# Kernel optimization log

Hardware: AMD Instinct MI355X
Metric: run time of the kernel (lower is better)

The kernel has to match this reference:

```python
import jax, jax.numpy as jnp
import numpy as np

H = 8
DA, DP, DK = 2048, 1024, 1024
B, N = 4, 2048
DOUT = 512
INNER = (DA + DP + DK) // H  # 512 = heads*dim_head


def setup_inputs() -> dict:
    key = jax.random.key(0)
    ks = jax.random.split(key, 7)
    x = jax.random.normal(ks[0], (B, N, DA + DP + DK), jnp.float32)
    mask = jax.random.randint(ks[1], (B, 1, N, N), 0, 2, jnp.int32)
    W_a = jax.random.normal(ks[2], (3 * DA // H, DA), jnp.float32) * (DA ** -0.5)
    W_p = jax.random.normal(ks[3], (3 * DP // H, DP), jnp.float32) * (DP ** -0.5)
    W_k = jax.random.normal(ks[4], (3 * DK // H, DK), jnp.float32) * (DK ** -0.5)
    W_out = jax.random.normal(ks[5], (DOUT, INNER), jnp.float32) * (INNER ** -0.5)
    b_out = jnp.zeros((DOUT,), jnp.float32)
    return {"x": x, "W_a": W_a, "W_p": W_p, "W_k": W_k,
            "W_out": W_out, "b_out": b_out, "mask": mask}


def _heads(t):  # [b, n, h*d] -> [b, h, n, d]
    b, n, hd = t.shape
    return t.reshape(b, n, H, hd // H).transpose(0, 2, 1, 3)


def reference(x, W_a, W_p, W_k, W_out, b_out, mask):
    # three branch QKV projections (each branch sees its own slice of x)
    qkv_a = x[..., :DA] @ W_a.T                      # [b, n, 3*DA/H]
    qkv_p = x[..., DA:DA + DP] @ W_p.T               # [b, n, 3*DP/H]
    qkv_k = x[..., DA + DP:] @ W_k.T                 # [b, n, 3*DK/H]
    q_a, k_a, v_a = [_heads(t) for t in jnp.split(qkv_a, 3, axis=-1)]
    q_p, k_p, v_p = [_heads(t) for t in jnp.split(qkv_p, 3, axis=-1)]
    q_k, k_k, v_k = [_heads(t) for t in jnp.split(qkv_k, 3, axis=-1)]

    m = mask > 0                                     # [b, 1, n, n]
    neg = jnp.asarray(-1e10, x.dtype)

    def branch(q, k, d):
        dots = jnp.einsum('bhid,bhjd->bhij', q, k) * (d ** -0.5)
        return jax.nn.softmax(jnp.where(m, dots, neg), axis=-1)

    # betas = [1,1,1] normalized -> 1/3 each (the nn.Parameters are unused in fwd)
    attn = (branch(q_a, k_a, DA) + branch(q_p, k_p, DP) + branch(q_k, k_k, DK)) / 3.0

    v = jnp.concatenate([v_a, v_p, v_k], axis=-1)    # [b, h, n, INNER/H]
    out = jnp.einsum('bhij,bhjd->bhid', attn, v)     # [b, h, n, INNER/H]
    out = out.transpose(0, 2, 1, 3).reshape(x.shape[0], x.shape[1], INNER)
    return out @ W_out.T + b_out
```

## Files before the change

### kernel.cpp

```cpp
#include <hip/hip_runtime.h>
#include <hip/hip_bf16.h>

typedef __attribute__((ext_vector_type(8))) __bf16 bf16x8;
typedef __attribute__((ext_vector_type(4))) float f32x4;
typedef unsigned short u16;
typedef unsigned int u32;
typedef unsigned long long u64;

__device__ __forceinline__ u32 cvtpk(float lo, float hi) {
  u32 r;
  asm("v_cvt_pk_bf16_f32 %0, %1, %2" : "=v"(r) : "v"(lo), "v"(hi));
  return r;
}
__device__ __forceinline__ float rexp2(float x) {
  float r;
  asm("v_exp_f32 %0, %1" : "=v"(r) : "v"(x));
  return r;
}
__device__ __forceinline__ void gl_lds16(const void* g, void* l) {
  __builtin_amdgcn_global_load_lds((const __attribute__((address_space(1))) void*)g,
                                   (__attribute__((address_space(3))) void*)l, 16, 0, 0);
}

__global__ __launch_bounds__(256) void prep_kernel(
    const float* __restrict__ x, u16* __restrict__ xb,
    const float* __restrict__ Wa, const float* __restrict__ Wp,
    const float* __restrict__ Wk, const float* __restrict__ Wo,
    u16* __restrict__ Wab, u16* __restrict__ Wpb,
    u16* __restrict__ Wkb, u16* __restrict__ Wob,
    const int* __restrict__ mask, u64* __restrict__ bits, int xblocks) {
  int bid = blockIdx.x;
  if (bid < xblocks) {
    const int idx = (bid * 256 + threadIdx.x) * 16;
    const float4 a0 = *(const float4*)(x + idx);
    const float4 a1 = *(const float4*)(x + idx + 4);
    const float4 a2 = *(const float4*)(x + idx + 8);
    const float4 a3 = *(const float4*)(x + idx + 12);
    uint4 t0, t1;
    t0.x = cvtpk(a0.x, a0.y); t0.y = cvtpk(a0.z, a0.w);
    t0.z = cvtpk(a1.x, a1.y); t0.w = cvtpk(a1.z, a1.w);
    t1.x = cvtpk(a2.x, a2.y); t1.y = cvtpk(a2.z, a2.w);
    t1.z = cvtpk(a3.x, a3.y); t1.w = cvtpk(a3.z, a3.w);
    *(uint4*)(xb + idx) = t0;
    *(uint4*)(xb + idx + 8) = t1;
    return;
  }
  bid -= xblocks;
  if (bid < 2560) {
    const float* s; u16* d; int base;
    if (bid < 1536)      { s = Wa; d = Wab; base = bid; }
    else if (bid < 1920) { s = Wp; d = Wpb; base = bid - 1536; }
    else if (bid < 2304) { s = Wk; d = Wkb; base = bid - 1920; }
    else                 { s = Wo; d = Wob; base = bid - 2304; }
    const int idx = (base * 256 + threadIdx.x) * 4;
    const float4 v = *(const float4*)(s + idx);
    *(uint2*)(d + idx) = make_uint2(cvtpk(v.x, v.y), cvtpk(v.z, v.w));
    return;
  }
  bid -= 2560;
  const int lane = threadIdx.x & 63;
  const long long gw = (long long)bid * 4 + (threadIdx.x >> 6);
  const long long nwaves = 1024LL * 4;
  const long long nwords = 16777216LL / 64;
  for (long long i = gw; i < nwords; i += nwaves) {
    const int m = mask[i * 64 + lane];
    const u64 bal = __ballot(m > 0);
    if (lane == 0) bits[i] = bal;
  }
}

__device__ __forceinline__ void qkv_store(
    float v0, float v1, float v2, float v3, int m_base, int c,
    int dhs, int seg, float fs,
    u16* __restrict__ Qb, u16* __restrict__ Kb, u16* __restrict__ Vt) {
  const int which = c >> (3 + dhs);
  const float f = (which == 0) ? fs : 1.0f;
  const u32 r01 = cvtpk(v0 * f, v1 * f);
  const u32 r23 = cvtpk(v2 * f, v3 * f);
  const u16 bvv[4] = {(u16)r01, (u16)(r01 >> 16), (u16)r23, (u16)(r23 >> 16)};
  const int hd_mask = (8 << dhs) - 1;
  const int r = c & hd_mask;
  const int hh = r >> dhs;
  const int d = r & ((1 << dhs) - 1);
  #pragma unroll
  for (int j = 0; j < 4; ++j) {
    const int m = m_base + j;
    const int bb = m >> 11, n = m & 2047;
    const size_t bhn = (size_t)(bb * 8 + hh) * 2048 + n;
    const u16 bv = bvv[j];
    if (which == 0)      Qb[bhn * 64 + seg + d] = bv;
    else if (which == 1) Kb[bhn * 64 + seg + d] = bv;
    else {
      const int nk6 = n & 63;
      const int pos = ((nk6 >> 5) << 5) | (((nk6 & 15) >> 2) << 3)
                    | ((nk6 & 3) << 1) | ((nk6 >> 4) & 1);
      Vt[((size_t)(bb * 8 + hh) * 64 + seg + d) * 2048 + (n & ~63) + pos] = bv;
    }
  }
}

__global__ __launch_bounds__(256) void qkv_gemm_kernel(
    const u16* __restrict__ xb, const u16* __restrict__ Wa,
    const u16* __restrict__ Wp, const u16* __restrict__ Wk,
    u16* __restrict__ Qb, u16* __restrict__ Kb, u16* __restrict__ Vt) {
  __shared__ u16 lA[64 * 64];
  __shared__ u16 lB[128 * 64];

  const int tid = threadIdx.x;
  const int w = tid >> 6, l = tid & 63;
  const int lr = l & 15, lg = l >> 4;

  const int wg = blockIdx.x;
  const int xcd = wg & 7;
  const int q = wg >> 3;
  const int mtl = q / 12, nt = q % 12;
  const int mt = (xcd << 4) + mtl;

  const u16* W; int xoff, Kd, col0, dhs, seg;
  if (nt < 6)      { W = Wa; xoff = 0;    Kd = 2048; col0 = nt * 128;       dhs = 5; seg = 0;  }
  else if (nt < 9) { W = Wp; xoff = 2048; Kd = 1024; col0 = (nt - 6) * 128; dhs = 4; seg = 32; }
  else             { W = Wk; xoff = 3072; Kd = 1024; col0 = (nt - 9) * 128; dhs = 4; seg = 48; }
  const float qscale = (dhs == 5) ? 0.031880107f : 0.045084220f;

  const int m0 = mt * 64;
  f32x4 acc[4][2] = {};
  const int ubase = tid & ~63;

  const int nk = Kd >> 6;
  #pragma unroll 1
  for (int kt = 0; kt < nk; ++kt) {
    const int k0 = kt << 6;
    #pragma unroll
    for (int i = 0; i < 2; ++i) {
      const int ch = i * 256 + tid;
      const int row = ch >> 3, c8 = (ch & 7) << 3;
      gl_lds16(xb + (size_t)(m0 + row) * 4096 + xoff + k0 + c8,
               lA + (size_t)(i * 256 + ubase) * 8);
    }
    #pragma unroll
    for (int i = 0; i < 4; ++i) {
      const int ch = i * 256 + tid;
      const int row = ch >> 3, c8 = (ch & 7) << 3;
      gl_lds16(W + (size_t)(col0 + row) * Kd + k0 + c8,
               lB + (size_t)(i * 256 + ubase) * 8);
    }
    __syncthreads();
    bf16x8 af[4][2], bfr[2][2];
    #pragma unroll
    for (int mi = 0; mi < 4; ++mi) {
      af[mi][0] = *(const bf16x8*)(lA + (mi * 16 + lr) * 64 + lg * 8);
      af[mi][1] = *(const bf16x8*)(lA + (mi * 16 + lr) * 64 + 32 + lg * 8);
    }
    #pragma unroll
    for (int ni = 0; ni < 2; ++ni) {
      bfr[ni][0] = *(const bf16x8*)(lB + (w * 32 + ni * 16 + lr) * 64 + lg * 8);
      bfr[ni][1] = *(const bf16x8*)(lB + (w * 32 + ni * 16 + lr) * 64 + 32 + lg * 8);
    }
    #pragma unroll
    for (int mi = 0; mi < 4; ++mi)
      #pragma unroll
      for (int ni = 0; ni < 2; ++ni) {
        acc[mi][ni] = __builtin_amdgcn_mfma_f32_16x16x32_bf16(af[mi][0], bfr[ni][0], acc[mi][ni], 0, 0, 0);
        acc[mi][ni] = __builtin_amdgcn_mfma_f32_16x16x32_bf16(af[mi][1], bfr[ni][1], acc[mi][ni], 0, 0, 0);
      }
    __syncthreads();
  }

  #pragma unroll
  for (int mi = 0; mi < 4; ++mi)
    #pragma unroll
    for (int ni = 0; ni < 2; ++ni)
      qkv_store(acc[mi][ni][0], acc[mi][ni][1], acc[mi][ni][2], acc[mi][ni][3],
                m0 + mi * 16 + lg * 4, col0 + w * 32 + ni * 16 + lr,
                dhs, seg, qscale, Qb, Kb, Vt);
}

__global__ __launch_bounds__(256) void qkv_gemm_f32_kernel(
    const float* __restrict__ x, const u16* __restrict__ Wa,
    const u16* __restrict__ Wp, const u16* __restrict__ Wk,
    u16* __restrict__ Qb, u16* __restrict__ Kb, u16* __restrict__ Vt) {
  __shared__ u16 lA[128 * 64];
  __shared__ u16 lB[128 * 64];

  const int tid = threadIdx.x;
  const int w = tid >> 6, l = tid & 63;
  const int lr = l & 15, lg = l >> 4;
  const int wr = w >> 1, wc = w & 1;

  const int wg = blockIdx.x;
  const int xcd = wg & 7;
  const int q = wg >> 3;
  const int mtl = q / 12, nt = q % 12;
  const int mt = (xcd << 3) + mtl;

  const u16* W; int xoff, Kd, col0, dhs, seg;
  if (nt < 6)      { W = Wa; xoff = 0;    Kd = 2048; col0 = nt * 128;       dhs = 5; seg = 0;  }
  else if (nt < 9) { W = Wp; xoff = 2048; Kd = 1024; col0 = (nt - 6) * 128; dhs = 4; seg = 32; }
  else             { W = Wk; xoff = 3072; Kd = 1024; col0 = (nt - 9) * 128; dhs = 4; seg = 48; }
  const float qscale = (dhs == 5) ? 0.031880107f : 0.045084220f;

  const int m0 = mt * 128;
  f32x4 acc[4][4] = {};
  const int ubase = tid & ~63;

  const int nk = Kd >> 6;
  #pragma unroll 1
  for (int kt = 0; kt < nk; ++kt) {
    const int k0 = kt << 6;
    #pragma unroll
    for (int i = 0; i < 4; ++i) {
      const int ch = i * 256 + tid;
      const int row = ch >> 3, c8 = (ch & 7) << 3;
      const float* src = x + (size_t)(m0 + row) * 4096 + xoff + k0 + c8;
      const float4 a0 = *(const float4*)(src);
      const float4 a1 = *(const float4*)(src + 4);
      uint4 t;
      t.x = cvtpk(a0.x, a0.y); t.y = cvtpk(a0.z, a0.w);
      t.z = cvtpk(a1.x, a1.y); t.w = cvtpk(a1.z, a1.w);
      *(uint4*)(lA + (size_t)row * 64 + c8) = t;
    }
    #pragma unroll
    for (int i = 0; i < 4; ++i) {
      const int ch = i * 256 + tid;
      const int row = ch >> 3, c8 = (ch & 7) << 3;
      gl_lds16(W + (size_t)(col0 + row) * Kd + k0 + c8,
               lB + (size_t)(i * 256 + ubase) * 8);
    }
    __syncthreads();
    bf16x8 af[4][2], bfr[4][2];
    #pragma unroll
    for (int mi = 0; mi < 4; ++mi) {
      af[mi][0] = *(const bf16x8*)(lA + (wr * 64 + mi * 16 + lr) * 64 + lg * 8);
      af[mi][1] = *(const bf16x8*)(lA + (wr * 64 + mi * 16 + lr) * 64 + 32 + lg * 8);
    }
    #pragma unroll
    for (int ni = 0; ni < 4; ++ni) {
      bfr[ni][0] = *(const bf16x8*)(lB + (wc * 64 + ni * 16 + lr) * 64 + lg * 8);
      bfr[ni][1] = *(const bf16x8*)(lB + (wc * 64 + ni * 16 + lr) * 64 + 32 + lg * 8);
    }
    #pragma unroll
    for (int mi = 0; mi < 4; ++mi)
      #pragma unroll
      for (int ni = 0; ni < 4; ++ni) {
        acc[mi][ni] = __builtin_amdgcn_mfma_f32_16x16x32_bf16(af[mi][0], bfr[ni][0], acc[mi][ni], 0, 0, 0);
        acc[mi][ni] = __builtin_amdgcn_mfma_f32_16x16x32_bf16(af[mi][1], bfr[ni][1], acc[mi][ni], 0, 0, 0);
      }
    __syncthreads();
  }
  #pragma unroll
  for (int mi = 0; mi < 4; ++mi)
    #pragma unroll
    for (int ni = 0; ni < 4; ++ni)
      qkv_store(acc[mi][ni][0], acc[mi][ni][1], acc[mi][ni][2], acc[mi][ni][3],
                m0 + wr * 64 + mi * 16 + lg * 4, col0 + wc * 64 + ni * 16 + lr,
                dhs, seg, qscale, Qb, Kb, Vt);
}

__global__ __launch_bounds__(512) void attn_kernel(
    const u16* __restrict__ Qb, const u16* __restrict__ Kb,
    const u16* __restrict__ Vt, const u32* __restrict__ mbits,
    u16* __restrict__ aout) {
  struct SMem {
    u16 sK[2][64 * 64];
    u16 sV[2][64 * 64];
  };
  __shared__ SMem sm;

  const int tid = threadIdx.x;
  const int w = tid >> 6, l = tid & 63;
  const int lr = l & 15, lg = l >> 4;
  const int wg = blockIdx.x;
  const int xcd = wg & 7, rr0 = wg >> 3;
  const int bh = (xcd << 2) + (rr0 >> 4);
  const int qt = rr0 & 15;
  const int b = bh >> 3, h = bh & 7;
  const int q0 = qt << 7;
  const size_t bhN = (size_t)bh * 2048;
  const int ubase = tid & ~63;

  const u16* qrow = Qb + (bhN + q0 + w * 16 + lr) * 64;
  const bf16x8 qf_a  = *(const bf16x8*)(qrow + lg * 8);
  const bf16x8 qf_pk = *(const bf16x8*)(qrow + 32 + lg * 8);
  bf16x8 zero8 = {};
  const bf16x8 qf_p = (lg < 2) ? qf_pk : zero8;
  const bf16x8 qf_k = (lg < 2) ? zero8 : qf_pk;

  const u32* mptr = mbits + ((size_t)b * 2048 + q0 + w * 16 + lr) * 64;

  const int sr = tid >> 3, swd = tid & 7;
  const u16* kp = Kb + (bhN + sr) * 64 + (swd ^ (sr & 7)) * 8;
  const u16* vp = Vt + ((size_t)bh * 64 + sr) * 2048 + (swd ^ (sr & 7)) * 8;
  u16* dK[2] = { &sm.sK[0][0] + ubase * 8, &sm.sK[1][0] + ubase * 8 };
  u16* dV[2] = { &sm.sV[0][0] + ubase * 8, &sm.sV[1][0] + ubase * 8 };

  gl_lds16(kp, dK[0]);
  gl_lds16(vp, dV[0]);

  bf16x8 vones;
  #pragma unroll
  for (int e = 0; e < 8; ++e) vones[e] = __builtin_bit_cast(__bf16, (u16)0x3F80);

  f32x4 oacc[3][4] = {};
  f32x4 osum[3] = {};
  const int c4 = (lg << 2);
  const int xk = lr & 7;

  auto body = [&](int kt, int cur, bool st) {
    if (st) {
      gl_lds16(kp + (size_t)(kt + 1) * 4096, dK[cur ^ 1]);
      gl_lds16(vp + (size_t)(kt + 1) * 64, dV[cur ^ 1]);
      asm volatile("s_waitcnt vmcnt(2)" ::: "memory");
    } else {
      asm volatile("s_waitcnt vmcnt(0)" ::: "memory");
    }
    __builtin_amdgcn_sched_barrier(0);
    __builtin_amdgcn_s_barrier();

    const uint2 mk = *(const uint2*)(mptr + (kt << 1));
    u32 msk[4][2];
    #pragma unroll
    for (int j = 0; j < 4; ++j) {
      const int c = c4 + j;
      const u32 u0 = (mk.x >> c) & 0x00010001u;
      const u32 u1 = (mk.y >> c) & 0x00010001u;
      msk[j][0] = (u0 << 16) - u0;
      msk[j][1] = (u1 << 16) - u1;
    }

    bf16x8 vb[4][2];
    #pragma unroll
    for (int ct = 0; ct < 4; ++ct) {
      const u16* vrow = &sm.sV[cur][0] + (ct * 16 + lr) * 64;
      vb[ct][0] = *(const bf16x8*)(vrow + (lg ^ xk) * 8);
      vb[ct][1] = *(const bf16x8*)(vrow + ((lg + 4) ^ xk) * 8);
    }

    const f32x4 fz = {0.f, 0.f, 0.f, 0.f};
    auto softpv = [&](f32x4 (&sacc)[4], int s) {
      uint4 pw0, pw1;
      u32* w0 = (u32*)&pw0; u32* w1 = (u32*)&pw1;
      #pragma unroll
      for (int j = 0; j < 4; ++j) {
        w0[j] = cvtpk(rexp2(sacc[0][j]), rexp2(sacc[1][j])) & msk[j][0];
        w1[j] = cvtpk(rexp2(sacc[2][j]), rexp2(sacc[3][j])) & msk[j][1];
      }
      const bf16x8 pa0 = __builtin_bit_cast(bf16x8, pw0);
      const bf16x8 pa1 = __builtin_bit_cast(bf16x8, pw1);
      __builtin_amdgcn_s_setprio(1);
      #pragma unroll
      for (int ct = 0; ct < 4; ++ct) {
        oacc[s][ct] = __builtin_amdgcn_mfma_f32_16x16x32_bf16(pa0, vb[ct][0], oacc[s][ct], 0, 0, 0);
        oacc[s][ct] = __builtin_amdgcn_mfma_f32_16x16x32_bf16(pa1, vb[ct][1], oacc[s][ct], 0, 0, 0);
      }
      osum[s] = __builtin_amdgcn_mfma_f32_16x16x32_bf16(pa0, vones, osum[s], 0, 0, 0);
      osum[s] = __builtin_amdgcn_mfma_f32_16x16x32_bf16(pa1, vones, osum[s], 0, 0, 0);
      __builtin_amdgcn_s_setprio(0);
    };

    {
      f32x4 sacc[4];
      __builtin_amdgcn_s_setprio(1);
      #pragma unroll
      for (int t = 0; t < 4; ++t) {
        const bf16x8 kf = *(const bf16x8*)(&sm.sK[cur][0] + (t * 16 + lr) * 64 + ((lg ^ xk) * 8));
        sacc[t] = __builtin_amdgcn_mfma_f32_16x16x32_bf16(kf, qf_a, fz, 0, 0, 0);
      }
      __builtin_amdgcn_s_setprio(0);
      softpv(sacc, 0);
    }
    {
      f32x4 sacc[4];
      __builtin_amdgcn_s_setprio(1);
      #pragma unroll
      for (int t = 0; t < 4; ++t) {
        const bf16x8 kf = *(const bf16x8*)(&sm.sK[cur][0] + (t * 16 + lr) * 64 + (((lg + 4) ^ xk) * 8));
        sacc[t] = __builtin_amdgcn_mfma_f32_16x16x32_bf16(kf, qf_p, fz, 0, 0, 0);
      }
      __builtin_amdgcn_s_setprio(0);
      softpv(sacc, 1);
    }
    {
      f32x4 sacc[4];
      __builtin_amdgcn_s_setprio(1);
      #pragma unroll
      for (int t = 0; t < 4; ++t) {
        const bf16x8 kf = *(const bf16x8*)(&sm.sK[cur][0] + (t * 16 + lr) * 64 + (((lg + 4) ^ xk) * 8));
        sacc[t] = __builtin_amdgcn_mfma_f32_16x16x32_bf16(kf, qf_k, fz, 0, 0, 0);
      }
      __builtin_amdgcn_s_setprio(0);
      softpv(sacc, 2);
    }

    __builtin_amdgcn_s_barrier();
  };

  #pragma unroll 1
  for (int it = 0; it < 16; ++it) {
    body(2 * it, 0, true);
    body(2 * it + 1, 1, it < 15);
  }

  float linv[3][4];
  #pragma unroll
  for (int s = 0; s < 3; ++s)
    #pragma unroll
    for (int j = 0; j < 4; ++j)
      linv[s][j] = 1.0f / (3.0f * osum[s][j] + 1e-30f);

  #pragma unroll
  for (int ct = 0; ct < 4; ++ct) {
    float vj[4];
    #pragma unroll
    for (int j = 0; j < 4; ++j)
      vj[j] = oacc[0][ct][j] * linv[0][j]
            + oacc[1][ct][j] * linv[1][j]
            + oacc[2][ct][j] * linv[2][j];
    const u32 r01 = cvtpk(vj[0], vj[1]);
    const u32 r23 = cvtpk(vj[2], vj[3]);
    const u16 bvv[4] = {(u16)r01, (u16)(r01 >> 16), (u16)r23, (u16)(r23 >> 16)};
    #pragma unroll
    for (int j = 0; j < 4; ++j) {
      const int row = q0 + w * 16 + lg * 4 + j;
      const int col = h * 64 + ct * 16 + lr;
      aout[((size_t)b * 2048 + row) * 512 + col] = bvv[j];
    }
  }
}

__global__ __launch_bounds__(256) void out_gemm_kernel(
    const u16* __restrict__ A, const u16* __restrict__ Wo,
    const float* __restrict__ bias, float* __restrict__ out) {
  __shared__ u16 lA[64 * 64];
  __shared__ u16 lB[64 * 64];

  const int tid = threadIdx.x;
  const int w = tid >> 6, l = tid & 63;
  const int lr = l & 15, lg = l >> 4;

  const int wg = blockIdx.x;
  const int xcd = wg & 7;
  const int q = wg >> 3;
  const int mt = (xcd << 4) + (q >> 3);
  const int nt = q & 7;
  const int col0 = nt * 64;
  const int m0 = mt * 64;
  f32x4 acc[4] = {};
  const int ubase = tid & ~63;

  #pragma unroll 1
  for (int kt = 0; kt < 8; ++kt) {
    const int k0 = kt << 6;
    #pragma unroll
    for (int i = 0; i < 2; ++i) {
      const int ch = i * 256 + tid;
      const int row = ch >> 3, c8 = (ch & 7) << 3;
      gl_lds16(A + (size_t)(m0 + row) * 512 + k0 + c8, lA + (size_t)(i * 256 + ubase) * 8);
    }
    #pragma unroll
    for (int i = 0; i < 2; ++i) {
      const int ch = i * 256 + tid;
      const int row = ch >> 3, c8 = (ch & 7) << 3;
      gl_lds16(Wo + (size_t)(col0 + row) * 512 + k0 + c8, lB + (size_t)(i * 256 + ubase) * 8);
    }
    __syncthreads();
    bf16x8 af[4][2], bfr[2];
    #pragma unroll
    for (int mi = 0; mi < 4; ++mi) {
      af[mi][0] = *(const bf16x8*)(lA + (mi * 16 + lr) * 64 + lg * 8);
      af[mi][1] = *(const bf16x8*)(lA + (mi * 16 + lr) * 64 + 32 + lg * 8);
    }
    bfr[0] = *(const bf16x8*)(lB + (w * 16 + lr) * 64 + lg * 8);
    bfr[1] = *(const bf16x8*)(lB + (w * 16 + lr) * 64 + 32 + lg * 8);
    #pragma unroll
    for (int mi = 0; mi < 4; ++mi) {
      acc[mi] = __builtin_amdgcn_mfma_f32_16x16x32_bf16(af[mi][0], bfr[0], acc[mi], 0, 0, 0);
      acc[mi] = __builtin_amdgcn_mfma_f32_16x16x32_bf16(af[mi][1], bfr[1], acc[mi], 0, 0, 0);
    }
    __syncthreads();
  }

  const int c = col0 + w * 16 + lr;
  const float bv = bias[c];
  #pragma unroll
  for (int mi = 0; mi < 4; ++mi)
    #pragma unroll
    for (int j = 0; j < 4; ++j) {
      const int m = m0 + mi * 16 + lg * 4 + j;
      out[(size_t)m * 512 + c] = acc[mi][j] + bv;
    }
}

extern "C" void kernel_launch(void* const* d_in, const int* in_sizes, int n_in,
                              void* d_out, int out_size, void* d_ws, size_t ws_size,
                              hipStream_t stream) {
  const float* x    = (const float*)d_in[0];
  const float* Wa   = (const float*)d_in[1];
  const float* Wp   = (const float*)d_in[2];
  const float* Wk   = (const float*)d_in[3];
  const float* Wo   = (const float*)d_in[4];
  const float* bo   = (const float*)d_in[5];
  const int* mask   = (const int*)d_in[6];
  float* out = (float*)d_out;

  char* ws = (char*)d_ws;
  u16* Wab = (u16*)ws;
  u16* Wpb = (u16*)(ws + 3145728);
  u16* Wkb = (u16*)(ws + 3932160);
  u16* Wob = (u16*)(ws + 4718592);
  u16* Qb  = (u16*)(ws + 5242880);
  u16* Kb  = (u16*)(ws + 13631488);
  u16* Vt  = (u16*)(ws + 22020096);
  u64* Mb  = (u64*)(ws + 30408704);
  u16* Ao  = (u16*)(ws + 32505856);
  u16* xb  = (u16*)(ws + 40894464);

  const bool use_xb = ws_size >= (size_t)40894464 + 67108864;
  const int xblocks = use_xb ? 8192 : 0;

  prep_kernel<<<xblocks + 2560 + 1024, 256, 0, stream>>>(
      x, xb, Wa, Wp, Wk, Wo, Wab, Wpb, Wkb, Wob, mask, (u64*)Mb, xblocks);
  if (use_xb) {
    qkv_gemm_kernel<<<1536, 256, 0, stream>>>(xb, Wab, Wpb, Wkb, Qb, Kb, Vt);
  } else {
    qkv_gemm_f32_kernel<<<768, 256, 0, stream>>>(x, Wab, Wpb, Wkb, Qb, Kb, Vt);
  }
  attn_kernel<<<512, 512, 0, stream>>>(Qb, Kb, Vt, (const u32*)Mb, Ao);
  out_gemm_kernel<<<1024, 256, 0, stream>>>(Ao, Wob, bo, out);
}
```

Baseline: 289.9 us.

## Stage V tiles through LDS for coalesced stores and prefetch mask bits

In the bf16 QKV GEMM, tiles that produce V columns now write the permuted bf16 results into shared memory and then issue coalesced 16-byte row stores to the transposed Vt buffer. Before, each lane scattered 2-byte writes. The attention kernel also loads the next tile's mask bitfield one iteration early, alongside the K/V async loads, with the vmcnt wait adjusted to match, so mask-load latency is hidden. This adds an extra block barrier and LDS traffic for V tiles, and ties the waitcnt accounting to the order of the loads.

After: 267.9 us. -7.6%, faster.

```diff
diff --git a/kernel.cpp b/kernel.cpp
--- a/kernel.cpp
+++ b/kernel.cpp
@@ -20,6 +20,9 @@
 __device__ __forceinline__ void gl_lds16(const void* g, void* l) {
   __builtin_amdgcn_global_load_lds((const __attribute__((address_space(1))) void*)g,
                                    (__attribute__((address_space(3))) void*)l, 16, 0, 0);
+}
+__device__ __forceinline__ int sigma_inv(int n) {
+  return ((n >> 5) << 5) | (((n & 15) >> 2) << 3) | ((n & 3) << 1) | ((n >> 4) & 1);
 }
 
 __global__ __launch_bounds__(256) void prep_kernel(
@@ -69,10 +72,10 @@
   }
 }
 
-__device__ __forceinline__ void qkv_store(
+__device__ __forceinline__ void qk_store(
     float v0, float v1, float v2, float v3, int m_base, int c,
     int dhs, int seg, float fs,
-    u16* __restrict__ Qb, u16* __restrict__ Kb, u16* __restrict__ Vt) {
+    u16* __restrict__ Qb, u16* __restrict__ Kb) {
   const int which = c >> (3 + dhs);
   const float f = (which == 0) ? fs : 1.0f;
   const u32 r01 = cvtpk(v0 * f, v1 * f);
@@ -88,14 +91,8 @@
     const int bb = m >> 11, n = m & 2047;
     const size_t bhn = (size_t)(bb * 8 + hh) * 2048 + n;
     const u16 bv = bvv[j];
-    if (which == 0)      Qb[bhn * 64 + seg + d] = bv;
-    else if (which == 1) Kb[bhn * 64 + seg + d] = bv;
-    else {
-      const int nk6 = n & 63;
-      const int pos = ((nk6 >> 5) << 5) | (((nk6 & 15) >> 2) << 3)
-                    | ((nk6 & 3) << 1) | ((nk6 >> 4) & 1);
-      Vt[((size_t)(bb * 8 + hh) * 64 + seg + d) * 2048 + (n & ~63) + pos] = bv;
-    }
+    if (which == 0) Qb[bhn * 64 + seg + d] = bv;
+    else            Kb[bhn * 64 + seg + d] = bv;
   }
 }
 
@@ -103,8 +100,9 @@
     const u16* __restrict__ xb, const u16* __restrict__ Wa,
     const u16* __restrict__ Wp, const u16* __restrict__ Wk,
     u16* __restrict__ Qb, u16* __restrict__ Kb, u16* __restrict__ Vt) {
-  __shared__ u16 lA[64 * 64];
-  __shared__ u16 lB[128 * 64];
+  __shared__ u16 smem[64 * 64 + 128 * 64];
+  u16* lA = smem;
+  u16* lB = smem + 64 * 64;
 
   const int tid = threadIdx.x;
   const int w = tid >> 6, l = tid & 63;
@@ -121,6 +119,7 @@
   else if (nt < 9) { W = Wp; xoff = 2048; Kd = 1024; col0 = (nt - 6) * 128; dhs = 4; seg = 32; }
   else             { W = Wk; xoff = 3072; Kd = 1024; col0 = (nt - 9) * 128; dhs = 4; seg = 48; }
   const float qscale = (dhs == 5) ? 0.031880107f : 0.045084220f;
+  const bool isV = (nt == 4) | (nt == 5) | (nt == 8) | (nt == 11);
 
   const int m0 = mt * 64;
   f32x4 acc[4][2] = {};
@@ -166,13 +165,41 @@
     __syncthreads();
   }
 
-  #pragma unroll
-  for (int mi = 0; mi < 4; ++mi)
-    #pragma unroll
-    for (int ni = 0; ni < 2; ++ni)
-      qkv_store(acc[mi][ni][0], acc[mi][ni][1], acc[mi][ni][2], acc[mi][ni][3],
-                m0 + mi * 16 + lg * 4, col0 + w * 32 + ni * 16 + lr,
-                dhs, seg, qscale, Qb, Kb, Vt);
+  if (!isV) {
+    #pragma unroll
+    for (int mi = 0; mi < 4; ++mi)
+      #pragma unroll
+      for (int ni = 0; ni < 2; ++ni)
+        qk_store(acc[mi][ni][0], acc[mi][ni][1], acc[mi][ni][2], acc[mi][ni][3],
+                 m0 + mi * 16 + lg * 4, col0 + w * 32 + ni * 16 + lr,
+                 dhs, seg, qscale, Qb, Kb);
+  } else {
+    #pragma unroll
+    for (int mi = 0; mi < 4; ++mi)
+      #pragma unroll
+      for (int ni = 0; ni < 2; ++ni) {
+        const u32 r01 = cvtpk(acc[mi][ni][0], acc[mi][ni][1]);
+        const u32 r23 = cvtpk(acc[mi][ni][2], acc[mi][ni][3]);
+        const u16 bvv[4] = {(u16)r01, (u16)(r01 >> 16), (u16)r23, (u16)(r23 >> 16)};
+        const int cl = w * 32 + ni * 16 + lr;
+        #pragma unroll
+        for (int j = 0; j < 4; ++j) {
+          const int n = mi * 16 + lg * 4 + j;
+          smem[cl * 72 + sigma_inv(n)] = bvv[j];
+        }
+      }
+    __syncthreads();
+    const int c = tid >> 1, half = (tid & 1) << 5;
+    const int hd_mask = (8 << dhs) - 1;
+    const int r = (col0 + c) & hd_mask;
+    const int hh = r >> dhs, d = r & ((1 << dhs) - 1);
+    const int bb = m0 >> 11, n0v = m0 & 2047;
+    u16* dst = Vt + ((size_t)(bb * 8 + hh) * 64 + seg + d) * 2048 + n0v + half;
+    const u16* srcl = smem + c * 72 + half;
+    #pragma unroll
+    for (int e = 0; e < 4; ++e)
+      *(uint4*)(dst + e * 8) = *(const uint4*)(srcl + e * 8);
+  }
 }
 
 __global__ __launch_bounds__(256) void qkv_gemm_f32_kernel(
@@ -250,10 +277,28 @@
   #pragma unroll
   for (int mi = 0; mi < 4; ++mi)
     #pragma unroll
-    for (int ni = 0; ni < 4; ++ni)
-      qkv_store(acc[mi][ni][0], acc[mi][ni][1], acc[mi][ni][2], acc[mi][ni][3],
-                m0 + wr * 64 + mi * 16 + lg * 4, col0 + wc * 64 + ni * 16 + lr,
-                dhs, seg, qscale, Qb, Kb, Vt);
+    for (int ni = 0; ni < 4; ++ni) {
+      const int c = col0 + wc * 64 + ni * 16 + lr;
+      const int which = c >> (3 + dhs);
+      const float f = (which == 0) ? qscale : 1.0f;
+      const u32 r01 = cvtpk(acc[mi][ni][0] * f, acc[mi][ni][1] * f);
+      const u32 r23 = cvtpk(acc[mi][ni][2] * f, acc[mi][ni][3] * f);
+      const u16 bvv[4] = {(u16)r01, (u16)(r01 >> 16), (u16)r23, (u16)(r23 >> 16)};
+      const int hd_mask = (8 << dhs) - 1;
+      const int r = c & hd_mask;
+      const int hh = r >> dhs;
+      const int d = r & ((1 << dhs) - 1);
+      #pragma unroll
+      for (int j = 0; j < 4; ++j) {
+        const int m = m0 + wr * 64 + mi * 16 + lg * 4 + j;
+        const int bb = m >> 11, n = m & 2047;
+        const size_t bhn = (size_t)(bb * 8 + hh) * 2048 + n;
+        const u16 bv = bvv[j];
+        if (which == 0)      Qb[bhn * 64 + seg + d] = bv;
+        else if (which == 1) Kb[bhn * 64 + seg + d] = bv;
+        else Vt[((size_t)(bb * 8 + hh) * 64 + seg + d) * 2048 + (n & ~63) + sigma_inv(n & 63)] = bv;
+      }
+    }
 }
 
 __global__ __launch_bounds__(512) void attn_kernel(
@@ -293,6 +338,8 @@
   u16* dK[2] = { &sm.sK[0][0] + ubase * 8, &sm.sK[1][0] + ubase * 8 };
   u16* dV[2] = { &sm.sV[0][0] + ubase * 8, &sm.sV[1][0] + ubase * 8 };
 
+  uint2 mkA = *(const uint2*)(mptr);
+  uint2 mkB;
   gl_lds16(kp, dK[0]);
   gl_lds16(vp, dV[0]);
 
@@ -305,24 +352,24 @@
   const int c4 = (lg << 2);
   const int xk = lr & 7;
 
-  auto body = [&](int kt, int cur, bool st) {
+  auto body = [&](int kt, int cur, bool st, uint2 mkv, uint2* mknext) {
     if (st) {
+      *mknext = *(const uint2*)(mptr + ((kt + 1) << 1));
       gl_lds16(kp + (size_t)(kt + 1) * 4096, dK[cur ^ 1]);
       gl_lds16(vp + (size_t)(kt + 1) * 64, dV[cur ^ 1]);
-      asm volatile("s_waitcnt vmcnt(2)" ::: "memory");
+      asm volatile("s_waitcnt vmcnt(3)" ::: "memory");
     } else {
       asm volatile("s_waitcnt vmcnt(0)" ::: "memory");
     }
     __builtin_amdgcn_sched_barrier(0);
     __builtin_amdgcn_s_barrier();
 
-    const uint2 mk = *(const uint2*)(mptr + (kt << 1));
     u32 msk[4][2];
     #pragma unroll
     for (int j = 0; j < 4; ++j) {
       const int c = c4 + j;
-      const u32 u0 = (mk.x >> c) & 0x00010001u;
-      const u32 u1 = (mk.y >> c) & 0x00010001u;
+      const u32 u0 = (mkv.x >> c) & 0x00010001u;
+      const u32 u1 = (mkv.y >> c) & 0x00010001u;
       msk[j][0] = (u0 << 16) - u0;
       msk[j][1] = (u1 << 16) - u1;
     }
@@ -396,8 +443,8 @@
 
   #pragma unroll 1
   for (int it = 0; it < 16; ++it) {
-    body(2 * it, 0, true);
-    body(2 * it + 1, 1, it < 15);
+    body(2 * it, 0, true, mkA, &mkB);
+    body(2 * it + 1, 1, it < 15, mkB, &mkA);
   }
 
   float linv[3][4];
```
